# Kernel tuning notes

Measured on AMD Instinct MI355X. Metric: run time of the kernel, lower is better.

Reference implementation:

```python
import jax, jax.numpy as jnp
import numpy as np

CUTOFF = 5.2
BUCKETS_PER_CUTOFF = 1
BOX = 100.0
N_ATOMS = 100000
EXTRA_SPACE = 1e-5

# half-shell neighbor displacements: cartesian_prod(arange(-b,1)^3)[:-1] -> 7 vectors for b=1
_d1 = np.arange(-BUCKETS_PER_CUTOFF, 1)
DISPLACEMENTS = jnp.asarray(
    np.stack(np.meshgrid(_d1, _d1, _d1, indexing='ij'), axis=-1).reshape(-1, 3)[:-1],
    dtype=jnp.int32)  # (7, 3)
NUM_NEIGHBORS = DISPLACEMENTS.shape[0]


def setup_inputs() -> dict:
    key = jax.random.key(0)
    k1, _ = jax.random.split(key)
    # uniform in [0, 0.999*BOX) so fractional coordinates are strictly < 1
    coordinates = jax.random.uniform(k1, (1, N_ATOMS, 3), dtype=jnp.float32) * (BOX * 0.999)
    cell = jnp.eye(3, dtype=jnp.float32) * BOX
    return {"coordinates": coordinates, "cell": cell}


def _cumsum_from_zero(x):
    return jnp.concatenate([jnp.zeros((1,), x.dtype), jnp.cumsum(x[:-1])])


def reference(coordinates, cell):
    n_atoms = coordinates.shape[1]
    cell_diag = jnp.diagonal(cell)                       # (3,)
    bucket_length = CUTOFF / BUCKETS_PER_CUTOFF + EXTRA_SPACE
    grid = jnp.floor(cell_diag / bucket_length).astype(jnp.int32) + 1   # shape_buckets_grid (3,)
    total_buckets = int(grid[0] * grid[1] * grid[2])
    # faithful to source: [g1*g2, g1, 1]
    scaling = jnp.array([grid[1] * grid[2], grid[1], 1], dtype=jnp.int32)

    # fractionalize + main bucket vector/flat indices
    frac = coordinates / cell_diag.reshape(1, 1, -1)     # (1, N, 3)
    vec_idx = jnp.round(frac * (grid - 1).astype(frac.dtype)).astype(jnp.int32)  # (1, N, 3)
    flat = (vec_idx * scaling).sum(-1).reshape(-1)       # (N,) main_bucket_flat_index

    # image-index converters (stable argsort by bucket)
    imidx_from_atidx = jnp.argsort(flat)                 # jax argsort is stable
    atidx_from_imidx = jnp.argsort(imidx_from_atidx)

    # per-bucket counts / exclusive cumcounts
    counts = jnp.bincount(flat, length=total_buckets)
    cumcounts = _cumsum_from_zero(counts)
    max_in_bucket = int(counts.max())

    # ---- within-image pairs ----
    wp_idx = jnp.nonzero(counts > 1)[0]
    wp_count = counts[wp_idx]
    wp_cum = cumcounts[wp_idx]
    pu, pl = jnp.triu_indices(max_in_bucket, k=1)
    pairs = jnp.stack([pu, pl]).astype(jnp.int32)        # (2, P)
    # sort_along_row(row_for_sorting=1): key = upper + lower*max_in_bucket
    order = jnp.argsort(pairs[0] + pairs[1] * max_in_bucket)
    pairs = pairs[:, order]
    padded = pairs[None] + wp_cum.reshape(-1, 1, 1)      # (B, 2, P)
    padded = jnp.transpose(padded, (1, 0, 2)).reshape(2, -1)
    max_pairs = max_in_bucket * (max_in_bucket - 1) // 2
    mask = (jnp.arange(max_pairs)[None, :] < (wp_count * (wp_count - 1) // 2)[:, None]).reshape(-1)
    within_image_pairs = jnp.stack([padded[0][mask], padded[1][mask]])  # (2, n_pairs)

    # ---- between-image 'lower' indices ----
    neigh_vec = vec_idx[:, :, None, :] + DISPLACEMENTS   # (1, N, 7, 3)
    neigh_vec = jnp.mod(neigh_vec, grid)                 # pbc wrap of neighbor buckets
    neigh_flat = (neigh_vec * scaling).sum(-1)           # (1, N, 7)
    n_count = counts[neigh_flat]                         # (1, N, 7)
    n_cum = cumcounts[neigh_flat]                        # (1, N, 7)
    pad = jnp.broadcast_to(
        jnp.arange(max_in_bucket, dtype=n_cum.dtype).reshape(1, 1, 1, -1),
        (1, n_atoms, NUM_NEIGHBORS, max_in_bucket))      # (1, N, 7, M) -- dominant intermediate
    m = pad < n_count[..., None]
    lower_between = (pad + n_cum[..., None])[m]          # (n_between,)

    return within_image_pairs, lower_between, frac, imidx_from_atidx, atidx_from_imidx
```

## Files before the change

### kernel.cpp

```cpp
#include <hip/hip_runtime.h>
#include <hip/hip_bf16.h>

#define NB_MAX 8192
#define NTHR 256


__global__ __launch_bounds__(NTHR) void k_count(
    const float* __restrict__ coord,
    const float* __restrict__ cell,
    float* __restrict__ out_frac,
    int* __restrict__ pv,
    int* __restrict__ counts,
    int* __restrict__ scalars,
    int* __restrict__ cumc,
    int* __restrict__ pairoff,
    int n) {
  __shared__ int shA[4], shB[4];
  __shared__ int isLast;
  int t = threadIdx.x;
  int lane = t & 63, wid = t >> 6;
  int a = blockIdx.x * NTHR + t;

  float d0 = cell[0], d1 = cell[4], d2 = cell[8];
  const float bl = (float)(5.2 + 1e-05);
  int g0 = (int)floorf(d0 / bl) + 1;
  int g1 = (int)floorf(d1 / bl) + 1;
  int g2 = (int)floorf(d2 / bl) + 1;
  int g12 = g1 * g2;
  if (a == 0) {
    scalars[8] = g0; scalars[9] = g1; scalars[10] = g2;
    scalars[11] = g12; scalars[12] = g0 * g12;
  }
  if (a < n) {
    float x = coord[3 * a + 0], y = coord[3 * a + 1], z = coord[3 * a + 2];
    float fx = x / d0, fy = y / d1, fz = z / d2;
    out_frac[3 * a + 0] = fx;
    out_frac[3 * a + 1] = fy;
    out_frac[3 * a + 2] = fz;
    int v0 = (int)rintf(fx * (float)(g0 - 1));
    int v1 = (int)rintf(fy * (float)(g1 - 1));
    int v2 = (int)rintf(fz * (float)(g2 - 1));
    pv[a] = (v0 << 20) | (v1 << 10) | v2;
    atomicAdd(&counts[v0 * g12 + v1 * g1 + v2], 1);
  }

  __syncthreads();
  if (t == 0) {
    int old = __hip_atomic_fetch_add(&scalars[13], 1, __ATOMIC_RELAXED,
                                     __HIP_MEMORY_SCOPE_AGENT);
    isLast = (old == (int)gridDim.x - 1) ? 1 : 0;
  }
  __syncthreads();
  if (!isLast) return;

  int nb = g0 * g12;
  const int IT = NB_MAX / NTHR;
  int base2 = t * IT;
  int cv[IT];
  int lc = 0, lp = 0;
#pragma unroll
  for (int i = 0; i < IT; ++i) {
    int idx = base2 + i;
    int c = (idx < nb)
        ? __hip_atomic_load(&counts[idx], __ATOMIC_RELAXED, __HIP_MEMORY_SCOPE_AGENT)
        : 0;
    cv[i] = c;
    lc += c;
    lp += c * (c - 1) / 2;
  }
  int ic = lc, ip = lp;
  for (int off = 1; off < 64; off <<= 1) {
    int yc = __shfl_up(ic, off);
    int yp = __shfl_up(ip, off);
    if (lane >= off) { ic += yc; ip += yp; }
  }
  if (lane == 63) { shA[wid] = ic; shB[wid] = ip; }
  __syncthreads();
  if (wid == 0 && lane < 4) {
    int vc2 = shA[lane], vp2 = shB[lane];
    int sc2 = vc2, sp2 = vp2;
    for (int off = 1; off < 4; off <<= 1) {
      int yc = __shfl_up(sc2, off);
      int yp = __shfl_up(sp2, off);
      if (lane >= off) { sc2 += yc; sp2 += yp; }
    }
    shA[lane] = sc2 - vc2;
    shB[lane] = sp2 - vp2;
  }
  __syncthreads();
  int ec = shA[wid] + (ic - lc);
  int ep = shB[wid] + (ip - lp);
#pragma unroll
  for (int i = 0; i < IT; ++i) {
    int idx = base2 + i;
    if (idx < nb) { cumc[idx] = ec; pairoff[idx] = ep; }
    ec += cv[i];
    ep += cv[i] * (cv[i] - 1) / 2;
  }
  if (t == NTHR - 1) scalars[0] = ep;
}

__global__ __launch_bounds__(NTHR) void k_scatter(
    const int* __restrict__ pv,
    const int* __restrict__ cumc,
    const int* __restrict__ counts,
    int* __restrict__ scalars,
    int* __restrict__ fill,
    int* __restrict__ sorted,
    int* __restrict__ Oarr,
    int* __restrict__ blockpart,
    int* __restrict__ blockoff,
    int n) {
  __shared__ int shA[4];
  __shared__ int isLast;
  int t = threadIdx.x;
  int lane = t & 63, wid = t >> 6;
  int a = blockIdx.x * NTHR + t;
  int g0 = scalars[8], g1 = scalars[9], g2 = scalars[10], g12 = scalars[11];
  int S = 0;
  if (a < n) {
    int p = pv[a];
    int v0 = p >> 20, v1 = (p >> 10) & 1023, v2 = p & 1023;
    int b = v0 * g12 + v1 * g1 + v2;
    int pos = cumc[b] + atomicAdd(&fill[b], 1);
    sorted[pos] = a;
#pragma unroll
    for (int m = 0; m < 7; ++m) {
      int dx = ((m >> 2) & 1) ? 0 : -1;
      int dy = ((m >> 1) & 1) ? 0 : -1;
      int dz = (m & 1) ? 0 : -1;
      int nx = v0 + dx; if (nx < 0) nx += g0;
      int ny = v1 + dy; if (ny < 0) ny += g1;
      int nz = v2 + dz; if (nz < 0) nz += g2;
      S += counts[nx * g12 + ny * g1 + nz];
    }
  }
  int iv = S;
  for (int off = 1; off < 64; off <<= 1) {
    int y = __shfl_up(iv, off);
    if (lane >= off) iv += y;
  }
  if (lane == 63) shA[wid] = iv;
  __syncthreads();
  if (wid == 0 && lane < 4) {
    int v2 = shA[lane], s2 = v2;
    for (int off = 1; off < 4; off <<= 1) {
      int y = __shfl_up(s2, off);
      if (lane >= off) s2 += y;
    }
    shA[lane] = s2 - v2;
    if (lane == 3) {
      __hip_atomic_store(&blockpart[blockIdx.x], s2, __ATOMIC_RELAXED,
                         __HIP_MEMORY_SCOPE_AGENT);
    }
  }
  __syncthreads();
  if (a < n) Oarr[a] = shA[wid] + (iv - S);

  __syncthreads();
  if (t == 0) {
    int old = __hip_atomic_fetch_add(&scalars[14], 1, __ATOMIC_RELAXED,
                                     __HIP_MEMORY_SCOPE_AGENT);
    isLast = (old == (int)gridDim.x - 1) ? 1 : 0;
  }
  __syncthreads();
  if (!isLast) return;

  int nblocks = gridDim.x;
  const int IT = 2;
  int base2 = t * IT;
  int cv[IT];
  int ls = 0;
#pragma unroll
  for (int i = 0; i < IT; ++i) {
    int idx = base2 + i;
    int v = (idx < nblocks)
        ? __hip_atomic_load(&blockpart[idx], __ATOMIC_RELAXED, __HIP_MEMORY_SCOPE_AGENT)
        : 0;
    cv[i] = v;
    ls += v;
  }
  int il = ls;
  for (int off = 1; off < 64; off <<= 1) {
    int y = __shfl_up(il, off);
    if (lane >= off) il += y;
  }
  if (lane == 63) shA[wid] = il;
  __syncthreads();
  if (wid == 0 && lane < 4) {
    int v2 = shA[lane], s2 = v2;
    for (int off = 1; off < 4; off <<= 1) {
      int y = __shfl_up(s2, off);
      if (lane >= off) s2 += y;
    }
    shA[lane] = s2 - v2;
  }
  __syncthreads();
  int e = shA[wid] + (il - ls);
#pragma unroll
  for (int i = 0; i < IT; ++i) {
    int idx = base2 + i;
    if (idx < nblocks) blockoff[idx] = e;
    e += cv[i];
  }
}

__global__ __launch_bounds__(NTHR) void k_sortemit(
    const int* __restrict__ counts,
    const int* __restrict__ cumc,
    const int* __restrict__ pairoff,
    const int* __restrict__ scalars,
    int* __restrict__ sorted,
    const int* __restrict__ pv,
    const int* __restrict__ Oarr,
    const int* __restrict__ blockoff,
    float* __restrict__ out_im,
    float* __restrict__ out_at,
    float* __restrict__ out,
    int n) {
  int t = threadIdx.x;
  int lane = t & 63, wid = t >> 6;

  if (blockIdx.x < 2048) {
    int b = blockIdx.x * 4 + wid;
    int nb = scalars[12];
    if (b >= nb) return;
    int c = counts[b];
    if (c == 0) return;
    int s = cumc[b];
    if (c == 1) {
      if (lane == 0) {
        int aa = sorted[s];
        out_im[s] = (float)aa;
        out_at[aa] = (float)s;
      }
      return;
    }
    if (c <= 64) {
      int val = (lane < c) ? sorted[s + lane] : 0x7fffffff;
      int rank = 0;
      for (int j = 0; j < c; ++j) {
        int other = __shfl(val, j);
        rank += (other < val) ? 1 : 0;
      }
      if (lane < c) {
        sorted[s + rank] = val;
        out_im[s + rank] = (float)val;
        out_at[val] = (float)(s + rank);
      }
    } else if (lane == 0) {
      for (int i = 1; i < c; ++i) {
        int key = sorted[s + i];
        int j = i - 1;
        while (j >= 0 && sorted[s + j] > key) {
          sorted[s + j + 1] = sorted[s + j];
          --j;
        }
        sorted[s + j + 1] = key;
      }
      for (int i = 0; i < c; ++i) {
        int aa = sorted[s + i];
        out_im[s + i] = (float)aa;
        out_at[aa] = (float)(s + i);
      }
    }
    int off = pairoff[b];
    int P = scalars[0];
    int np = c * (c - 1) / 2;
    for (int k = lane; k < np; k += 64) {
      int l = (int)((1.0f + sqrtf(1.0f + 8.0f * (float)k)) * 0.5f);
      while (l * (l - 1) / 2 > k) --l;
      while ((l + 1) * l / 2 <= k) ++l;
      int u = k - l * (l - 1) / 2;
      out[off + k] = (float)(s + u);
      out[P + off + k] = (float)(s + l);
    }
    return;
  }

  int a = (blockIdx.x - 2048) * 16 + (t >> 4);
  int l16 = t & 15;
  if (a >= n) return;
  int g0 = scalars[8], g1 = scalars[9], g2 = scalars[10], g12 = scalars[11];
  int p = pv[a];
  int v0 = p >> 20, v1 = (p >> 10) & 1023, v2 = p & 1023;
  int segs[8];
  int cums[7];
  segs[0] = 0;
#pragma unroll
  for (int m = 0; m < 7; ++m) {
    int dx = ((m >> 2) & 1) ? 0 : -1;
    int dy = ((m >> 1) & 1) ? 0 : -1;
    int dz = (m & 1) ? 0 : -1;
    int nx = v0 + dx; if (nx < 0) nx += g0;
    int ny = v1 + dy; if (ny < 0) ny += g1;
    int nz = v2 + dz; if (nz < 0) nz += g2;
    int nb_ = nx * g12 + ny * g1 + nz;
    cums[m] = cumc[nb_];
    segs[m + 1] = segs[m] + counts[nb_];
  }
  int S = segs[7];
  long base = 2L * (long)scalars[0] + (long)blockoff[a >> 8] + (long)Oarr[a];
  for (int q = l16; q < S; q += 16) {
    int v = cums[0] + q;
#pragma unroll
    for (int m = 1; m < 7; ++m) {
      if (q >= segs[m]) v = cums[m] + (q - segs[m]);
    }
    out[base + q] = (float)v;
  }
}

extern "C" void kernel_launch(void* const* d_in, const int* in_sizes, int n_in,
                              void* d_out, int out_size, void* d_ws, size_t ws_size,
                              hipStream_t stream) {
  const float* coord = (const float*)d_in[0];
  const float* cell = (const float*)d_in[1];
  float* out = (float*)d_out;
  int n = in_sizes[0] / 3;

  int* W = (int*)d_ws;
  int* counts = W;
  int* fill = W + NB_MAX;
  int* scalars = W + 2 * NB_MAX;
  int* cumc = W + 2 * NB_MAX + 16;
  int* pairoff = cumc + NB_MAX;
  int* pv = pairoff + NB_MAX;
  int* sorted = pv + n;
  int* Oarr = sorted + n;
  int* blockpart = Oarr + n;
  int* blockoff = blockpart + 1024;

  float* out_frac = out + (out_size - 5 * n);
  float* out_im = out + (out_size - 2 * n);
  float* out_at = out + (out_size - n);

  int nblocks = (n + NTHR - 1) / NTHR;
  int eblocks = (n + 15) / 16;

  hipMemsetAsync(d_ws, 0, (size_t)(2 * NB_MAX + 16) * sizeof(int), stream);

  k_count<<<nblocks, NTHR, 0, stream>>>(coord, cell, out_frac, pv, counts, scalars,
                                        cumc, pairoff, n);
  k_scatter<<<nblocks, NTHR, 0, stream>>>(pv, cumc, counts, scalars, fill, sorted,
                                          Oarr, blockpart, blockoff, n);
  k_sortemit<<<2048 + eblocks, NTHR, 0, stream>>>(counts, cumc, pairoff, scalars,
                                                  sorted, pv, Oarr, blockoff,
                                                  out_im, out_at, out, n);
}
```

Measured before the change: 116.9 us.

## Fuse between-bucket emission into scatter using decoupled lookback scan

The between-image index emission moves from the sort kernel into the scatter kernel. Per-atom neighbour bucket offsets are kept in shared memory, and the global exclusive offset comes from a single-pass decoupled lookback scan instead of a last-block scan plus a separate emit pass. This removes the Oarr/blockoff round trip through global memory and the re-gathering of neighbour counts. In exchange it adds serial dependence between blocks through lookback spinning and uses more shared memory per block, which may lower occupancy.

```diff
diff --git a/kernel.cpp b/kernel.cpp
--- a/kernel.cpp
+++ b/kernel.cpp
@@ -1,5 +1,4 @@
 #include <hip/hip_runtime.h>
-#include <hip/hip_bf16.h>
 
 #define NB_MAX 8192
 #define NTHR 256
@@ -100,23 +99,27 @@
   if (t == NTHR - 1) scalars[0] = ep;
 }
 
-__global__ __launch_bounds__(NTHR) void k_scatter(
+__global__ __launch_bounds__(NTHR) void k_scatter_emit(
     const int* __restrict__ pv,
     const int* __restrict__ cumc,
     const int* __restrict__ counts,
-    int* __restrict__ scalars,
+    const int* __restrict__ scalars,
     int* __restrict__ fill,
     int* __restrict__ sorted,
-    int* __restrict__ Oarr,
-    int* __restrict__ blockpart,
-    int* __restrict__ blockoff,
+    unsigned long long* __restrict__ lookback,
+    float* __restrict__ out,
     int n) {
   __shared__ int shA[4];
-  __shared__ int isLast;
+  __shared__ int Lsegs[NTHR][7];
+  __shared__ int Lcums[NTHR][7];
+  __shared__ int Lexcl[NTHR];
+  __shared__ int sh_agg, sh_E;
   int t = threadIdx.x;
   int lane = t & 63, wid = t >> 6;
-  int a = blockIdx.x * NTHR + t;
+  int bid = blockIdx.x;
+  int a = bid * NTHR + t;
   int g0 = scalars[8], g1 = scalars[9], g2 = scalars[10], g12 = scalars[11];
+
   int S = 0;
   if (a < n) {
     int p = pv[a];
@@ -124,6 +127,7 @@
     int b = v0 * g12 + v1 * g1 + v2;
     int pos = cumc[b] + atomicAdd(&fill[b], 1);
     sorted[pos] = a;
+    int seg = 0;
 #pragma unroll
     for (int m = 0; m < 7; ++m) {
       int dx = ((m >> 2) & 1) ? 0 : -1;
@@ -132,9 +136,17 @@
       int nx = v0 + dx; if (nx < 0) nx += g0;
       int ny = v1 + dy; if (ny < 0) ny += g1;
       int nz = v2 + dz; if (nz < 0) nz += g2;
-      S += counts[nx * g12 + ny * g1 + nz];
-    }
-  }
+      int nb_ = nx * g12 + ny * g1 + nz;
+      Lcums[t][m] = cumc[nb_];
+      seg += counts[nb_];
+      Lsegs[t][m] = seg;
+    }
+    S = seg;
+  } else {
+#pragma unroll
+    for (int m = 0; m < 7; ++m) { Lsegs[t][m] = 0; Lcums[t][m] = 0; }
+  }
+
   int iv = S;
   for (int off = 1; off < 64; off <<= 1) {
     int y = __shfl_up(iv, off);
@@ -143,171 +155,157 @@
   if (lane == 63) shA[wid] = iv;
   __syncthreads();
   if (wid == 0 && lane < 4) {
-    int v2 = shA[lane], s2 = v2;
+    int v2_ = shA[lane], s2 = v2_;
     for (int off = 1; off < 4; off <<= 1) {
       int y = __shfl_up(s2, off);
       if (lane >= off) s2 += y;
     }
-    shA[lane] = s2 - v2;
-    if (lane == 3) {
-      __hip_atomic_store(&blockpart[blockIdx.x], s2, __ATOMIC_RELAXED,
+    shA[lane] = s2 - v2_;
+  }
+  __syncthreads();
+  int eoff = shA[wid] + (iv - S);
+  Lexcl[t] = eoff;
+  if (t == NTHR - 1) sh_agg = eoff + S;
+  __syncthreads();
+
+  if (wid == 0) {
+    unsigned long long agg = (unsigned long long)(unsigned)sh_agg;
+    if (lane == 0) {
+      unsigned long long w = (agg << 32) | (bid == 0 ? 2ull : 1ull);
+      __hip_atomic_store(&lookback[bid], w, __ATOMIC_RELAXED,
                          __HIP_MEMORY_SCOPE_AGENT);
     }
-  }
-  __syncthreads();
-  if (a < n) Oarr[a] = shA[wid] + (iv - S);
-
-  __syncthreads();
-  if (t == 0) {
-    int old = __hip_atomic_fetch_add(&scalars[14], 1, __ATOMIC_RELAXED,
-                                     __HIP_MEMORY_SCOPE_AGENT);
-    isLast = (old == (int)gridDim.x - 1) ? 1 : 0;
-  }
-  __syncthreads();
-  if (!isLast) return;
-
-  int nblocks = gridDim.x;
-  const int IT = 2;
-  int base2 = t * IT;
-  int cv[IT];
-  int ls = 0;
-#pragma unroll
-  for (int i = 0; i < IT; ++i) {
-    int idx = base2 + i;
-    int v = (idx < nblocks)
-        ? __hip_atomic_load(&blockpart[idx], __ATOMIC_RELAXED, __HIP_MEMORY_SCOPE_AGENT)
-        : 0;
-    cv[i] = v;
-    ls += v;
-  }
-  int il = ls;
-  for (int off = 1; off < 64; off <<= 1) {
-    int y = __shfl_up(il, off);
-    if (lane >= off) il += y;
-  }
-  if (lane == 63) shA[wid] = il;
-  __syncthreads();
-  if (wid == 0 && lane < 4) {
-    int v2 = shA[lane], s2 = v2;
-    for (int off = 1; off < 4; off <<= 1) {
-      int y = __shfl_up(s2, off);
-      if (lane >= off) s2 += y;
-    }
-    shA[lane] = s2 - v2;
-  }
-  __syncthreads();
-  int e = shA[wid] + (il - ls);
-#pragma unroll
-  for (int i = 0; i < IT; ++i) {
-    int idx = base2 + i;
-    if (idx < nblocks) blockoff[idx] = e;
-    e += cv[i];
+    asm volatile("" ::: "memory");
+    int E = 0;
+    if (bid > 0) {
+      int startp = bid - 1;
+      for (;;) {
+        int p = startp - lane;
+        unsigned long long u = (2ull);
+        int flag = 2;
+        if (p >= 0) {
+          do {
+            u = __hip_atomic_load(&lookback[p], __ATOMIC_RELAXED,
+                                  __HIP_MEMORY_SCOPE_AGENT);
+            flag = (int)(u & 3ull);
+          } while (flag == 0);
+        }
+        int val = (int)(u >> 32);
+        unsigned long long m2 = __ballot(flag == 2);
+        if (m2 != 0ull) {
+          int d = __ffsll((long long)m2) - 1;
+          int contrib = (lane <= d) ? val : 0;
+          for (int off = 1; off < 64; off <<= 1) contrib += __shfl_xor(contrib, off);
+          E += contrib;
+          break;
+        } else {
+          int contrib = val;
+          for (int off = 1; off < 64; off <<= 1) contrib += __shfl_xor(contrib, off);
+          E += contrib;
+          startp -= 64;
+        }
+      }
+      asm volatile("" ::: "memory");
+      if (lane == 0) {
+        unsigned long long w =
+            (((unsigned long long)(unsigned)(E + sh_agg)) << 32) | 2ull;
+        __hip_atomic_store(&lookback[bid], w, __ATOMIC_RELAXED,
+                           __HIP_MEMORY_SCOPE_AGENT);
+      }
+    }
+    if (lane == 0) sh_E = E;
+  }
+  __syncthreads();
+
+  int E = sh_E;
+  long obase = 2L * (long)scalars[0] + (long)E;
+  int l16 = t & 15;
+  int sub = t >> 4;
+#pragma unroll 1
+  for (int pass = 0; pass < 16; ++pass) {
+    int ai = pass * 16 + sub;
+    int s1 = Lsegs[ai][0], s2 = Lsegs[ai][1], s3 = Lsegs[ai][2], s4 = Lsegs[ai][3];
+    int s5 = Lsegs[ai][4], s6 = Lsegs[ai][5], s7 = Lsegs[ai][6];
+    int c0 = Lcums[ai][0], c1 = Lcums[ai][1], c2 = Lcums[ai][2], c3 = Lcums[ai][3];
+    int c4 = Lcums[ai][4], c5 = Lcums[ai][5], c6 = Lcums[ai][6];
+    long base = obase + (long)Lexcl[ai];
+    for (int q = l16; q < s7; q += 16) {
+      int v = c0 + q;
+      if (q >= s1) v = c1 + (q - s1);
+      if (q >= s2) v = c2 + (q - s2);
+      if (q >= s3) v = c3 + (q - s3);
+      if (q >= s4) v = c4 + (q - s4);
+      if (q >= s5) v = c5 + (q - s5);
+      if (q >= s6) v = c6 + (q - s6);
+      out[base + q] = (float)v;
+    }
   }
 }
 
-__global__ __launch_bounds__(NTHR) void k_sortemit(
+__global__ __launch_bounds__(NTHR) void k_sort(
     const int* __restrict__ counts,
     const int* __restrict__ cumc,
     const int* __restrict__ pairoff,
     const int* __restrict__ scalars,
     int* __restrict__ sorted,
-    const int* __restrict__ pv,
-    const int* __restrict__ Oarr,
-    const int* __restrict__ blockoff,
     float* __restrict__ out_im,
     float* __restrict__ out_at,
-    float* __restrict__ out,
-    int n) {
+    float* __restrict__ out) {
   int t = threadIdx.x;
   int lane = t & 63, wid = t >> 6;
 
-  if (blockIdx.x < 2048) {
-    int b = blockIdx.x * 4 + wid;
-    int nb = scalars[12];
-    if (b >= nb) return;
-    int c = counts[b];
-    if (c == 0) return;
-    int s = cumc[b];
-    if (c == 1) {
-      if (lane == 0) {
-        int aa = sorted[s];
-        out_im[s] = (float)aa;
-        out_at[aa] = (float)s;
+  int b = blockIdx.x * 4 + wid;
+  int nb = scalars[12];
+  if (b >= nb) return;
+  int c = counts[b];
+  if (c == 0) return;
+  int s = cumc[b];
+  if (c == 1) {
+    if (lane == 0) {
+      int aa = sorted[s];
+      out_im[s] = (float)aa;
+      out_at[aa] = (float)s;
+    }
+    return;
+  }
+  if (c <= 64) {
+    int val = (lane < c) ? sorted[s + lane] : 0x7fffffff;
+    int rank = 0;
+    for (int j = 0; j < c; ++j) {
+      int other = __shfl(val, j);
+      rank += (other < val) ? 1 : 0;
+    }
+    if (lane < c) {
+      sorted[s + rank] = val;
+      out_im[s + rank] = (float)val;
+      out_at[val] = (float)(s + rank);
+    }
+  } else if (lane == 0) {
+    for (int i = 1; i < c; ++i) {
+      int key = sorted[s + i];
+      int j = i - 1;
+      while (j >= 0 && sorted[s + j] > key) {
+        sorted[s + j + 1] = sorted[s + j];
+        --j;
       }
-      return;
-    }
-    if (c <= 64) {
-      int val = (lane < c) ? sorted[s + lane] : 0x7fffffff;
-      int rank = 0;
-      for (int j = 0; j < c; ++j) {
-        int other = __shfl(val, j);
-        rank += (other < val) ? 1 : 0;
-      }
-      if (lane < c) {
-        sorted[s + rank] = val;
-        out_im[s + rank] = (float)val;
-        out_at[val] = (float)(s + rank);
-      }
-    } else if (lane == 0) {
-      for (int i = 1; i < c; ++i) {
-        int key = sorted[s + i];
-        int j = i - 1;
-        while (j >= 0 && sorted[s + j] > key) {
-          sorted[s + j + 1] = sorted[s + j];
-          --j;
-        }
-        sorted[s + j + 1] = key;
-      }
-      for (int i = 0; i < c; ++i) {
-        int aa = sorted[s + i];
-        out_im[s + i] = (float)aa;
-        out_at[aa] = (float)(s + i);
-      }
-    }
-    int off = pairoff[b];
-    int P = scalars[0];
-    int np = c * (c - 1) / 2;
-    for (int k = lane; k < np; k += 64) {
-      int l = (int)((1.0f + sqrtf(1.0f + 8.0f * (float)k)) * 0.5f);
-      while (l * (l - 1) / 2 > k) --l;
-      while ((l + 1) * l / 2 <= k) ++l;
-      int u = k - l * (l - 1) / 2;
-      out[off + k] = (float)(s + u);
-      out[P + off + k] = (float)(s + l);
-    }
-    return;
-  }
-
-  int a = (blockIdx.x - 2048) * 16 + (t >> 4);
-  int l16 = t & 15;
-  if (a >= n) return;
-  int g0 = scalars[8], g1 = scalars[9], g2 = scalars[10], g12 = scalars[11];
-  int p = pv[a];
-  int v0 = p >> 20, v1 = (p >> 10) & 1023, v2 = p & 1023;
-  int segs[8];
-  int cums[7];
-  segs[0] = 0;
-#pragma unroll
-  for (int m = 0; m < 7; ++m) {
-    int dx = ((m >> 2) & 1) ? 0 : -1;
-    int dy = ((m >> 1) & 1) ? 0 : -1;
-    int dz = (m & 1) ? 0 : -1;
-    int nx = v0 + dx; if (nx < 0) nx += g0;
-    int ny = v1 + dy; if (ny < 0) ny += g1;
-    int nz = v2 + dz; if (nz < 0) nz += g2;
-    int nb_ = nx * g12 + ny * g1 + nz;
-    cums[m] = cumc[nb_];
-    segs[m + 1] = segs[m] + counts[nb_];
-  }
-  int S = segs[7];
-  long base = 2L * (long)scalars[0] + (long)blockoff[a >> 8] + (long)Oarr[a];
-  for (int q = l16; q < S; q += 16) {
-    int v = cums[0] + q;
-#pragma unroll
-    for (int m = 1; m < 7; ++m) {
-      if (q >= segs[m]) v = cums[m] + (q - segs[m]);
-    }
-    out[base + q] = (float)v;
+      sorted[s + j + 1] = key;
+    }
+    for (int i = 0; i < c; ++i) {
+      int aa = sorted[s + i];
+      out_im[s + i] = (float)aa;
+      out_at[aa] = (float)(s + i);
+    }
+  }
+  int off = pairoff[b];
+  int P = scalars[0];
+  int np = c * (c - 1) / 2;
+  for (int k = lane; k < np; k += 64) {
+    int l = (int)((1.0f + sqrtf(1.0f + 8.0f * (float)k)) * 0.5f);
+    while (l * (l - 1) / 2 > k) --l;
+    while ((l + 1) * l / 2 <= k) ++l;
+    int u = k - l * (l - 1) / 2;
+    out[off + k] = (float)(s + u);
+    out[P + off + k] = (float)(s + l);
   }
 }
 
@@ -323,28 +321,25 @@
   int* counts = W;
   int* fill = W + NB_MAX;
   int* scalars = W + 2 * NB_MAX;
-  int* cumc = W + 2 * NB_MAX + 16;
+  unsigned long long* lookback =
+      (unsigned long long*)(W + 2 * NB_MAX + 16);
+  int* cumc = W + 2 * NB_MAX + 16 + 1024;
   int* pairoff = cumc + NB_MAX;
   int* pv = pairoff + NB_MAX;
   int* sorted = pv + n;
-  int* Oarr = sorted + n;
-  int* blockpart = Oarr + n;
-  int* blockoff = blockpart + 1024;
 
   float* out_frac = out + (out_size - 5 * n);
   float* out_im = out + (out_size - 2 * n);
   float* out_at = out + (out_size - n);
 
   int nblocks = (n + NTHR - 1) / NTHR;
-  int eblocks = (n + 15) / 16;
-
-  hipMemsetAsync(d_ws, 0, (size_t)(2 * NB_MAX + 16) * sizeof(int), stream);
+
+  hipMemsetAsync(d_ws, 0, (size_t)(2 * NB_MAX + 16 + 1024) * sizeof(int), stream);
 
   k_count<<<nblocks, NTHR, 0, stream>>>(coord, cell, out_frac, pv, counts, scalars,
                                         cumc, pairoff, n);
-  k_scatter<<<nblocks, NTHR, 0, stream>>>(pv, cumc, counts, scalars, fill, sorted,
-                                          Oarr, blockpart, blockoff, n);
-  k_sortemit<<<2048 + eblocks, NTHR, 0, stream>>>(counts, cumc, pairoff, scalars,
-                                                  sorted, pv, Oarr, blockoff,
-                                                  out_im, out_at, out, n);
+  k_scatter_emit<<<nblocks, NTHR, 0, stream>>>(pv, cumc, counts, scalars, fill,
+                                               sorted, lookback, out, n);
+  k_sort<<<2048, NTHR, 0, stream>>>(counts, cumc, pairoff, scalars, sorted,
+                                    out_im, out_at, out);
 }
```

Measured after the change: 122.6 us. 4.9% more time.
